# Optimization experiments

Measured on AMD Instinct MI355X. Metric: run time of the kernel, lower is better.

## Reference

```python
import jax, jax.numpy as jnp
import numpy as np

DIM = 1024
HEADS = 16
HEAD_DIM = DIM // HEADS
HIDDEN = int(DIM * 4.0)
EPS = 1e-5


def setup_inputs() -> dict:
    key = jax.random.key(0)
    ks = jax.random.split(key, 12)
    s = 0.02
    return {
        "x": jax.random.normal(ks[0], (4, 2048, DIM), dtype=jnp.float32),
        "ln1_g": jnp.ones((DIM,), jnp.float32),
        "ln1_b": jnp.zeros((DIM,), jnp.float32),
        "ln2_g": jnp.ones((DIM,), jnp.float32),
        "ln2_b": jnp.zeros((DIM,), jnp.float32),
        "w_qkv": jax.random.normal(ks[1], (DIM, 3 * DIM), jnp.float32) * s,
        "b_qkv": jnp.zeros((3 * DIM,), jnp.float32),
        "w_proj": jax.random.normal(ks[2], (DIM, DIM), jnp.float32) * s,
        "b_proj": jnp.zeros((DIM,), jnp.float32),
        "w_fc1": jax.random.normal(ks[3], (DIM, HIDDEN), jnp.float32) * s,
        "b_fc1": jnp.zeros((HIDDEN,), jnp.float32),
        "w_fc2": jax.random.normal(ks[4], (HIDDEN, DIM), jnp.float32) * s,
        "b_fc2": jnp.zeros((DIM,), jnp.float32),
    }


def _layernorm(x, g, b):
    mu = jnp.mean(x, axis=-1, keepdims=True)
    var = jnp.mean(jnp.square(x - mu), axis=-1, keepdims=True)
    return (x - mu) * jax.lax.rsqrt(var + EPS) * g + b


def reference(x, ln1_g, ln1_b, ln2_g, ln2_b, w_qkv, b_qkv, w_proj, b_proj,
              w_fc1, b_fc1, w_fc2, b_fc2):
    B, N, C = x.shape
    # --- attention branch (pre-norm) ---
    h = _layernorm(x, ln1_g, ln1_b)
    qkv = (h @ w_qkv + b_qkv).reshape(B, N, 3, HEADS, HEAD_DIM)
    q, k, v = qkv[:, :, 0], qkv[:, :, 1], qkv[:, :, 2]  # [B,N,H,D]
    scale = HEAD_DIM ** -0.5
    attn = jnp.einsum("bnhd,bmhd->bhnm", q, k) * scale
    attn = jax.nn.softmax(attn, axis=-1)
    o = jnp.einsum("bhnm,bmhd->bnhd", attn, v).reshape(B, N, C)
    x = x + (o @ w_proj + b_proj)
    # --- MLP branch (pre-norm) ---
    h = _layernorm(x, ln2_g, ln2_b)
    h = jax.nn.gelu(h @ w_fc1 + b_fc1, approximate=False)
    x = x + (h @ w_fc2 + b_fc2)
    return x
```

## Files before the change

### kernel.cpp

```cpp
#include <hip/hip_runtime.h>
#include <stdint.h>

#define DIMC   1024
#define HEADS  16
#define HD     64
#define HIDDEN 4096
#define BATCH  4
#define SEQ    2048
#define ROWS   (BATCH*SEQ)

typedef unsigned short u16;
typedef __attribute__((ext_vector_type(8))) short bf16x8;
typedef __attribute__((ext_vector_type(4))) float f32x4;
typedef __attribute__((address_space(1))) void* gas_ptr;
typedef __attribute__((address_space(3))) void* las_ptr;

struct u16x4s { u16 x, y, z, w; };

__device__ __forceinline__ u16 f2bf(float f) {
    union { float f; uint32_t u; } x; x.f = f;
    uint32_t r = (x.u + 0x7FFFu + ((x.u >> 16) & 1u)) >> 16;
    return (u16)r;
}
__device__ __forceinline__ u16 f2bf_rtz(float f) {
    union { float f; uint32_t u; } x; x.f = f;
    return (u16)(x.u >> 16);
}

__device__ __forceinline__ bf16x8 ld_frag(const u16* p) {
    return *(const bf16x8*)p;
}

__global__ __launch_bounds__(256) void transpose_bf16(const float* __restrict__ w,
                                                      u16* __restrict__ wt, int K, int N) {
    __shared__ float tile[32][33];
    int bx = blockIdx.x * 32, by = blockIdx.y * 32;
    int tx = threadIdx.x & 31, ty = threadIdx.x >> 5;
#pragma unroll
    for (int i = 0; i < 32; i += 8)
        tile[ty + i][tx] = w[(size_t)(by + ty + i) * N + bx + tx];
    __syncthreads();
#pragma unroll
    for (int i = 0; i < 32; i += 8)
        wt[(size_t)(bx + ty + i) * K + by + tx] = f2bf(tile[tx][ty + i]);
}

__global__ __launch_bounds__(256) void transpose_v(const u16* __restrict__ vb,
                                                   u16* __restrict__ vt) {
    __shared__ u16 t[64][72];
    const int bh = blockIdx.y;
    const int n0 = blockIdx.x * 64;
    const int tid = threadIdx.x;
    const int r = tid >> 3, c = (tid & 7) * 8;
    const u16* src = vb + ((size_t)bh * SEQ + n0) * HD;
#pragma unroll
    for (int half = 0; half < 2; half++) {
        int n = half * 32 + r;
        *(bf16x8*)&t[n][c] = *(const bf16x8*)(src + (size_t)n * HD + c);
    }
    __syncthreads();
    u16* dst = vt + (size_t)bh * HD * SEQ + n0;
#pragma unroll
    for (int half = 0; half < 2; half++) {
        int d = half * 32 + r;
        u16 tmp[8];
#pragma unroll
        for (int j = 0; j < 8; j++) tmp[j] = t[c + j][d];
        *(bf16x8*)(dst + (size_t)d * SEQ + c) = *(const bf16x8*)tmp;
    }
}

__global__ __launch_bounds__(256) void ln_fwd(const float* __restrict__ x,
                                              const float* __restrict__ g,
                                              const float* __restrict__ bta,
                                              u16* __restrict__ out) {
    __shared__ float red[8];
    int row = blockIdx.x, tid = threadIdx.x;
    int wave = tid >> 6, lane = tid & 63;
    const float4 v = ((const float4*)(x + (size_t)row * DIMC))[tid];
    float s  = v.x + v.y + v.z + v.w;
    float s2 = v.x * v.x + v.y * v.y + v.z * v.z + v.w * v.w;
#pragma unroll
    for (int off = 1; off < 64; off <<= 1) {
        s  += __shfl_xor(s,  off, 64);
        s2 += __shfl_xor(s2, off, 64);
    }
    if (lane == 0) { red[wave] = s; red[4 + wave] = s2; }
    __syncthreads();
    s  = red[0] + red[1] + red[2] + red[3];
    s2 = red[4] + red[5] + red[6] + red[7];
    float mu = s * (1.f / DIMC);
    float rs = rsqrtf(s2 * (1.f / DIMC) - mu * mu + 1e-5f);
    float4 gv = ((const float4*)g)[tid];
    float4 bv = ((const float4*)bta)[tid];
    u16x4s o;
    o.x = f2bf((v.x - mu) * rs * gv.x + bv.x);
    o.y = f2bf((v.y - mu) * rs * gv.y + bv.y);
    o.z = f2bf((v.z - mu) * rs * gv.z + bv.z);
    o.w = f2bf((v.w - mu) * rs * gv.w + bv.w);
    *(u16x4s*)(out + (size_t)row * DIMC + tid * 4) = o;
}

#define EPI_F32_RESID 0
#define EPI_BF16      1
#define EPI_BF16_GELU 2
#define EPI_QKV       3

__global__ __launch_bounds__(256) void gemm_bt(
    const u16* __restrict__ A, const u16* __restrict__ Bt,
    const float* __restrict__ bias, const float* __restrict__ resid,
    float* __restrict__ outf, u16* __restrict__ outb,
    int M, int N, int K, int epi,
    u16* __restrict__ qb, u16* __restrict__ kbuf, u16* __restrict__ vb) {
    __shared__ u16 As[128 * 32];
    __shared__ u16 Bs[128 * 32];
    const int tid  = threadIdx.x;
    const int wave = tid >> 6, lane = tid & 63;
    const int quad = lane >> 4, l16 = lane & 15;
    const int bm0 = blockIdx.y * 128, bn0 = blockIdx.x * 128;
    const int wm = (wave >> 1) * 64, wn = (wave & 1) * 64;

    f32x4 acc[4][4];
#pragma unroll
    for (int i = 0; i < 4; i++)
#pragma unroll
        for (int j = 0; j < 4; j++) acc[i][j] = (f32x4){0.f, 0.f, 0.f, 0.f};

    const int sr  = lane >> 2;
    const int scs = ((lane & 3) ^ ((lane >> 3) & 3)) * 8;
    const u16* gA = A  + (size_t)(bm0 + wave * 32 + sr) * K + scs;
    const u16* gB = Bt + (size_t)(bn0 + wave * 32 + sr) * K + scs;
    u16* sA0 = As + wave * 1024;
    u16* sB0 = Bs + wave * 1024;

    const int sw = (l16 >> 1) & 3;

    for (int k0 = 0; k0 < K; k0 += 32) {
        __syncthreads();
        __builtin_amdgcn_global_load_lds((gas_ptr)(gA + k0),                  (las_ptr)(sA0),       16, 0, 0);
        __builtin_amdgcn_global_load_lds((gas_ptr)(gA + k0 + 16 * (size_t)K), (las_ptr)(sA0 + 512), 16, 0, 0);
        __builtin_amdgcn_global_load_lds((gas_ptr)(gB + k0),                  (las_ptr)(sB0),       16, 0, 0);
        __builtin_amdgcn_global_load_lds((gas_ptr)(gB + k0 + 16 * (size_t)K), (las_ptr)(sB0 + 512), 16, 0, 0);
        __syncthreads();

        bf16x8 af[4], bfr[4];
#pragma unroll
        for (int t = 0; t < 4; t++) {
            af[t]  = ld_frag(As + (wm + t * 16 + l16) * 32 + (quad ^ sw) * 8);
            bfr[t] = ld_frag(Bs + (wn + t * 16 + l16) * 32 + (quad ^ sw) * 8);
        }
#pragma unroll
        for (int i = 0; i < 4; i++)
#pragma unroll
            for (int j = 0; j < 4; j++)
                acc[i][j] = __builtin_amdgcn_mfma_f32_16x16x32_bf16(af[i], bfr[j], acc[i][j], 0, 0, 0);
    }

#pragma unroll
    for (int j = 0; j < 4; j++) {
        int gn = bn0 + wn + j * 16 + l16;
        float bv = bias[gn];
#pragma unroll
        for (int i = 0; i < 4; i++) {
            int gmb = bm0 + wm + i * 16 + quad * 4;
#pragma unroll
            for (int r = 0; r < 4; r++) {
                int gm = gmb + r;
                float v = acc[i][j][r] + bv;
                if (epi == EPI_F32_RESID) {
                    outf[(size_t)gm * N + gn] = resid[(size_t)gm * N + gn] + v;
                } else if (epi == EPI_BF16) {
                    outb[(size_t)gm * N + gn] = f2bf(v);
                } else if (epi == EPI_BF16_GELU) {
                    float gg = 0.5f * v * (1.f + erff(v * 0.70710678118654752f));
                    outb[(size_t)gm * N + gn] = f2bf(gg);
                } else {
                    int which = gn >> 10, hd_ = gn & 1023;
                    int h = hd_ >> 6, d = hd_ & 63;
                    int b = gm >> 11, n = gm & 2047;
                    u16* base = (which == 0) ? qb : (which == 1) ? kbuf : vb;
                    size_t bh = (size_t)(b * HEADS + h);
                    base[(bh * SEQ + n) * HD + d] = f2bf(v);
                }
            }
        }
    }
}

__global__ __launch_bounds__(256) void attn_fwd(const u16* __restrict__ q,
                                                const u16* __restrict__ kk,
                                                const u16* __restrict__ vt,
                                                u16* __restrict__ o) {
    __shared__ u16 Ks[64 * 64];
    __shared__ u16 Vs[64 * 64];
    __shared__ u16 Pb[4][32 * 72];
    const int tid = threadIdx.x;
    const int wave = tid >> 6, lane = tid & 63;
    const int quad = lane >> 4, l16 = lane & 15;
    const int bh = blockIdx.y;
    const int b = bh >> 4, h = bh & 15;
    const int q0 = blockIdx.x * 128 + wave * 32;

    const u16* Q  = q  + (size_t)bh * SEQ * HD;
    const u16* Kp = kk + (size_t)bh * SEQ * HD;
    const u16* VT = vt + (size_t)bh * HD * SEQ;

    bf16x8 qf[2][2];
#pragma unroll
    for (int rb = 0; rb < 2; rb++)
#pragma unroll
        for (int hf = 0; hf < 2; hf++)
            qf[rb][hf] = ld_frag(Q + (size_t)(q0 + rb * 16 + l16) * HD + hf * 32 + quad * 8);

    f32x4 of[2][4], lsum[2];
#pragma unroll
    for (int rb = 0; rb < 2; rb++) {
        lsum[rb] = (f32x4){0.f, 0.f, 0.f, 0.f};
#pragma unroll
        for (int dc = 0; dc < 4; dc++) of[rb][dc] = (f32x4){0.f, 0.f, 0.f, 0.f};
    }

    const short one_bf = (short)0x3F80;
    const bf16x8 ones = {one_bf, one_bf, one_bf, one_bf, one_bf, one_bf, one_bf, one_bf};

    const int srow = lane >> 3;
    const int schk = (lane & 7) ^ srow;
    const u16* gK = Kp + (size_t)(wave * 16 + srow) * HD + schk * 8;
    const u16* gV = VT + (size_t)(wave * 16 + srow) * SEQ + schk * 8;
    u16* sK = Ks + (wave * 16) * 64;
    u16* sV = Vs + (wave * 16) * 64;
    u16* pb = Pb[wave];
    const int sw = l16 & 7;

    for (int kb = 0; kb < SEQ; kb += 64) {
        __syncthreads();
        __builtin_amdgcn_global_load_lds((gas_ptr)(gK + (size_t)kb * HD),            (las_ptr)(sK),            16, 0, 0);
        __builtin_amdgcn_global_load_lds((gas_ptr)(gK + (size_t)(kb + 8) * HD),      (las_ptr)(sK + 8 * 64),   16, 0, 0);
        __builtin_amdgcn_global_load_lds((gas_ptr)(gV + kb),                         (las_ptr)(sV),            16, 0, 0);
        __builtin_amdgcn_global_load_lds((gas_ptr)(gV + kb + 8 * (size_t)SEQ),       (las_ptr)(sV + 8 * 64),   16, 0, 0);
        __syncthreads();

        f32x4 s[2][4];
#pragma unroll
        for (int kblk = 0; kblk < 4; kblk++) {
            const u16* krow = Ks + (kblk * 16 + l16) * 64;
            bf16x8 kf0 = ld_frag(krow + ((quad ^ sw) * 8));
            bf16x8 kf1 = ld_frag(krow + (((4 + quad) ^ sw) * 8));
            s[0][kblk] = __builtin_amdgcn_mfma_f32_16x16x32_bf16(qf[0][0], kf0, (f32x4){0.f,0.f,0.f,0.f}, 0, 0, 0);
            s[0][kblk] = __builtin_amdgcn_mfma_f32_16x16x32_bf16(qf[0][1], kf1, s[0][kblk], 0, 0, 0);
            s[1][kblk] = __builtin_amdgcn_mfma_f32_16x16x32_bf16(qf[1][0], kf0, (f32x4){0.f,0.f,0.f,0.f}, 0, 0, 0);
            s[1][kblk] = __builtin_amdgcn_mfma_f32_16x16x32_bf16(qf[1][1], kf1, s[1][kblk], 0, 0, 0);
        }

#pragma unroll
        for (int rb = 0; rb < 2; rb++)
#pragma unroll
            for (int kblk = 0; kblk < 4; kblk++)
#pragma unroll
                for (int r = 0; r < 4; r++) {
                    float p = __expf(s[rb][kblk][r] * 0.125f);
                    pb[(rb * 16 + quad * 4 + r) * 72 + kblk * 16 + l16] = f2bf_rtz(p);
                }

        bf16x8 pf[2][2];
#pragma unroll
        for (int rb = 0; rb < 2; rb++)
#pragma unroll
            for (int hf = 0; hf < 2; hf++)
                pf[rb][hf] = ld_frag(pb + (rb * 16 + l16) * 72 + hf * 32 + quad * 8);

#pragma unroll
        for (int hf = 0; hf < 2; hf++) {
#pragma unroll
            for (int dc = 0; dc < 4; dc++) {
                const u16* vrow = Vs + (dc * 16 + l16) * 64;
                bf16x8 vf = ld_frag(vrow + (((hf * 4 + quad) ^ sw) * 8));
                of[0][dc] = __builtin_amdgcn_mfma_f32_16x16x32_bf16(pf[0][hf], vf, of[0][dc], 0, 0, 0);
                of[1][dc] = __builtin_amdgcn_mfma_f32_16x16x32_bf16(pf[1][hf], vf, of[1][dc], 0, 0, 0);
            }
            lsum[0] = __builtin_amdgcn_mfma_f32_16x16x32_bf16(pf[0][hf], ones, lsum[0], 0, 0, 0);
            lsum[1] = __builtin_amdgcn_mfma_f32_16x16x32_bf16(pf[1][hf], ones, lsum[1], 0, 0, 0);
        }
    }

#pragma unroll
    for (int rb = 0; rb < 2; rb++) {
        float rl[4];
#pragma unroll
        for (int r = 0; r < 4; r++) rl[r] = 1.f / lsum[rb][r];
#pragma unroll
        for (int dc = 0; dc < 4; dc++)
#pragma unroll
            for (int r = 0; r < 4; r++) {
                float val = of[rb][dc][r] * rl[r];
                o[(size_t)(b * SEQ + q0 + rb * 16 + quad * 4 + r) * DIMC + h * HD + dc * 16 + l16] = f2bf(val);
            }
    }
}

extern "C" void kernel_launch(void* const* d_in, const int* in_sizes, int n_in,
                              void* d_out, int out_size, void* d_ws, size_t ws_size,
                              hipStream_t stream) {
    (void)in_sizes; (void)n_in; (void)out_size; (void)ws_size;
    const float* x      = (const float*)d_in[0];
    const float* ln1_g  = (const float*)d_in[1];
    const float* ln1_b  = (const float*)d_in[2];
    const float* ln2_g  = (const float*)d_in[3];
    const float* ln2_b  = (const float*)d_in[4];
    const float* w_qkv  = (const float*)d_in[5];
    const float* b_qkv  = (const float*)d_in[6];
    const float* w_proj = (const float*)d_in[7];
    const float* b_proj = (const float*)d_in[8];
    const float* w_fc1  = (const float*)d_in[9];
    const float* b_fc1  = (const float*)d_in[10];
    const float* w_fc2  = (const float*)d_in[11];
    const float* b_fc2  = (const float*)d_in[12];

    char* ws = (char*)d_ws;
    u16*   wqkvT  = (u16*)(ws);
    u16*   wprojT = (u16*)(ws + 6291456);
    u16*   wfc1T  = (u16*)(ws + 8388608);
    u16*   wfc2T  = (u16*)(ws + 16777216);
    u16*   hb     = (u16*)(ws + 25165824);
    float* x1     = (float*)(ws + 41943040);
    u16*   vb     = (u16*)(ws + 41943040);
    u16*   qb     = (u16*)(ws + 75497472);
    u16*   kb     = (u16*)(ws + 92274688);
    u16*   vtb    = (u16*)(ws + 109051904);
    u16*   ob     = (u16*)(ws + 125829120);
    u16*   a1     = qb;

    dim3 blk(256);
    transpose_bf16<<<dim3(3072 / 32, 1024 / 32), blk, 0, stream>>>(w_qkv,  wqkvT,  1024, 3072);
    transpose_bf16<<<dim3(1024 / 32, 1024 / 32), blk, 0, stream>>>(w_proj, wprojT, 1024, 1024);
    transpose_bf16<<<dim3(4096 / 32, 1024 / 32), blk, 0, stream>>>(w_fc1,  wfc1T,  1024, 4096);
    transpose_bf16<<<dim3(1024 / 32, 4096 / 32), blk, 0, stream>>>(w_fc2,  wfc2T,  4096, 1024);

    ln_fwd<<<dim3(ROWS), blk, 0, stream>>>(x, ln1_g, ln1_b, hb);

    gemm_bt<<<dim3(3072 / 128, ROWS / 128), blk, 0, stream>>>(
        hb, wqkvT, b_qkv, nullptr, nullptr, nullptr, ROWS, 3072, 1024, EPI_QKV, qb, kb, vb);

    transpose_v<<<dim3(SEQ / 64, BATCH * HEADS), blk, 0, stream>>>(vb, vtb);

    attn_fwd<<<dim3(SEQ / 128, BATCH * HEADS), blk, 0, stream>>>(qb, kb, vtb, ob);

    gemm_bt<<<dim3(1024 / 128, ROWS / 128), blk, 0, stream>>>(
        ob, wprojT, b_proj, x, x1, nullptr, ROWS, 1024, 1024, EPI_F32_RESID, nullptr, nullptr, nullptr);

    ln_fwd<<<dim3(ROWS), blk, 0, stream>>>(x1, ln2_g, ln2_b, hb);

    gemm_bt<<<dim3(4096 / 128, ROWS / 128), blk, 0, stream>>>(
        hb, wfc1T, b_fc1, nullptr, nullptr, a1, ROWS, 4096, 1024, EPI_BF16_GELU, nullptr, nullptr, nullptr);

    gemm_bt<<<dim3(1024 / 128, ROWS / 128), blk, 0, stream>>>(
        a1, wfc2T, b_fc2, x1, (float*)d_out, nullptr, ROWS, 1024, 4096, EPI_F32_RESID, nullptr, nullptr, nullptr);
}
```

Measured before the change: 660.8 us.

## Double-buffer A tiles in LDS and load B fragments directly from global

The GEMM main loop now uses a K-step of 64 with double-buffered LDS for the A tile, prefetching the next A tile asynchronously while MFMAs run on the current one. The B operand bypasses LDS: each wave loads its B fragments straight from global memory into registers, ping-ponged between two register sets so the next step's loads overlap compute. This is meant to hide global latency and drop one barrier per iteration. The costs are higher register pressure, possibly lower occupancy, and uncoalesced, redundant global reads of B across the two waves that share a column block. The loop also assumes K is a multiple of 128, since nt is processed in pairs.

```diff
diff --git a/kernel.cpp b/kernel.cpp
--- a/kernel.cpp
+++ b/kernel.cpp
@@ -112,8 +112,7 @@
     float* __restrict__ outf, u16* __restrict__ outb,
     int M, int N, int K, int epi,
     u16* __restrict__ qb, u16* __restrict__ kbuf, u16* __restrict__ vb) {
-    __shared__ u16 As[128 * 32];
-    __shared__ u16 Bs[128 * 32];
+    __shared__ u16 As[2][2][128 * 32];
     const int tid  = threadIdx.x;
     const int wave = tid >> 6, lane = tid & 63;
     const int quad = lane >> 4, l16 = lane & 15;
@@ -128,32 +127,58 @@
 
     const int sr  = lane >> 2;
     const int scs = ((lane & 3) ^ ((lane >> 3) & 3)) * 8;
-    const u16* gA = A  + (size_t)(bm0 + wave * 32 + sr) * K + scs;
-    const u16* gB = Bt + (size_t)(bn0 + wave * 32 + sr) * K + scs;
-    u16* sA0 = As + wave * 1024;
-    u16* sB0 = Bs + wave * 1024;
-
+    const u16* gA = A + (size_t)(bm0 + wave * 32 + sr) * K + scs;
     const int sw = (l16 >> 1) & 3;
 
-    for (int k0 = 0; k0 < K; k0 += 32) {
+    const u16* pB = Bt + (size_t)(bn0 + wn + l16) * K + quad * 8;
+
+    auto stageA = [&](int buf, int k0) {
+#pragma unroll
+        for (int p = 0; p < 2; p++) {
+            u16* s = (u16*)As[buf][p] + wave * 1024;
+            const u16* g = gA + k0 + p * 32;
+            __builtin_amdgcn_global_load_lds((gas_ptr)(g),                    (las_ptr)(s),       16, 0, 0);
+            __builtin_amdgcn_global_load_lds((gas_ptr)(g + 16 * (size_t)K),   (las_ptr)(s + 512), 16, 0, 0);
+        }
+    };
+    auto loadB = [&](bf16x8 (&dst)[8], int k0) {
+#pragma unroll
+        for (int ks = 0; ks < 2; ks++)
+#pragma unroll
+            for (int t = 0; t < 4; t++)
+                dst[ks * 4 + t] = ld_frag(pB + (size_t)t * 16 * K + k0 + ks * 32);
+    };
+
+    bf16x8 b0[8], b1[8];
+    stageA(0, 0);
+    loadB(b0, 0);
+
+    const int nt = K >> 6;
+    auto body = [&](bf16x8 (&bc)[8], bf16x8 (&bn)[8], int t2, int buf) {
         __syncthreads();
-        __builtin_amdgcn_global_load_lds((gas_ptr)(gA + k0),                  (las_ptr)(sA0),       16, 0, 0);
-        __builtin_amdgcn_global_load_lds((gas_ptr)(gA + k0 + 16 * (size_t)K), (las_ptr)(sA0 + 512), 16, 0, 0);
-        __builtin_amdgcn_global_load_lds((gas_ptr)(gB + k0),                  (las_ptr)(sB0),       16, 0, 0);
-        __builtin_amdgcn_global_load_lds((gas_ptr)(gB + k0 + 16 * (size_t)K), (las_ptr)(sB0 + 512), 16, 0, 0);
-        __syncthreads();
-
-        bf16x8 af[4], bfr[4];
-#pragma unroll
-        for (int t = 0; t < 4; t++) {
-            af[t]  = ld_frag(As + (wm + t * 16 + l16) * 32 + (quad ^ sw) * 8);
-            bfr[t] = ld_frag(Bs + (wn + t * 16 + l16) * 32 + (quad ^ sw) * 8);
-        }
+        bf16x8 af[2][4];
+#pragma unroll
+        for (int p = 0; p < 2; p++)
+#pragma unroll
+            for (int t = 0; t < 4; t++)
+                af[p][t] = ld_frag((u16*)As[buf][p] + (wm + t * 16 + l16) * 32 + (quad ^ sw) * 8);
+        if (t2 + 1 < nt) stageA(buf ^ 1, (t2 + 1) << 6);
 #pragma unroll
         for (int i = 0; i < 4; i++)
 #pragma unroll
             for (int j = 0; j < 4; j++)
-                acc[i][j] = __builtin_amdgcn_mfma_f32_16x16x32_bf16(af[i], bfr[j], acc[i][j], 0, 0, 0);
+                acc[i][j] = __builtin_amdgcn_mfma_f32_16x16x32_bf16(af[0][i], bc[j], acc[i][j], 0, 0, 0);
+        if (t2 + 1 < nt) loadB(bn, (t2 + 1) << 6);
+#pragma unroll
+        for (int i = 0; i < 4; i++)
+#pragma unroll
+            for (int j = 0; j < 4; j++)
+                acc[i][j] = __builtin_amdgcn_mfma_f32_16x16x32_bf16(af[1][i], bc[4 + j], acc[i][j], 0, 0, 0);
+    };
+
+    for (int t2 = 0; t2 < nt; t2 += 2) {
+        body(b0, b1, t2,     0);
+        body(b1, b0, t2 + 1, 1);
     }
 
 #pragma unroll
```

After: 1.125 ms. +70.3%, slower.
